# Performance work log

Measured on AMD Instinct MI355X. Metric: run time of the kernel, lower is better.

## Reference

```python
import jax, jax.numpy as jnp
import numpy as np

B = 8
RESOLUTIONS = [65, 129, 257, 513, 1025]
NUM_POINTS = [0, 4096, 16384, 65536, 262144]
CLIP_MIN = -1e9
FINAL = 1025          # last resolution (both axes)
B_MIN, B_MAX = -1.0, 1.0
BALANCE = 0.5


def setup_inputs() -> dict:
    key = jax.random.key(0)
    k1, k2, k3, k4 = jax.random.split(key, 4)
    return {
        "w1": jax.random.normal(k1, (2, 256), jnp.float32),
        "b1": jax.random.normal(k2, (256,), jnp.float32),
        "w2": jax.random.normal(k3, (256, 1), jnp.float32),
        "b2": jax.random.normal(k4, (1,), jnp.float32),
    }


def _interp_bilinear_ac(x, H, W):
    """F.interpolate(..., mode='bilinear', align_corners=True). x: [B, C, h, w]."""
    b, c, h, w = x.shape
    ys = jnp.linspace(0.0, h - 1.0, H)
    xs = jnp.linspace(0.0, w - 1.0, W)
    y0 = jnp.floor(ys).astype(jnp.int32)
    y1 = jnp.minimum(y0 + 1, h - 1)
    wy = ys - y0
    x0 = jnp.floor(xs).astype(jnp.int32)
    x1 = jnp.minimum(x0 + 1, w - 1)
    wx = xs - x0
    # interpolate rows, then columns
    top = x[:, :, y0, :] * (1.0 - wy)[None, None, :, None] + x[:, :, y1, :] * wy[None, None, :, None]
    return top[:, :, :, x0] * (1.0 - wx) + top[:, :, :, x1] * wx


def _batch_eval(coords, w1, b1, w2, b2):
    """coords: [B, N, 2] in final-resolution pixel space (align_corners=False mapping).
    Returns occupancy [B, N] (C == 1)."""
    coords2d = coords / FINAL + 0.5 / FINAL                 # normalize to [0, 1]
    p = coords2d * (B_MAX - B_MIN) + B_MIN                  # [B, N, 2] in world coords
    h = jax.nn.relu(jnp.einsum('bnd,dh->bnh', p, w1) + b1)  # [B, N, 256]
    occ = jax.nn.sigmoid(jnp.einsum('bnh,ho->bno', h, w2) + b2)
    return occ[..., 0]


def reference(w1, b1, w2, b2):
    occ = None
    for i, res in enumerate(RESOLUTIONS):
        if i == 0:
            # init_coords: grid of res x res points spanning [0, FINAL-1]
            xs = jnp.linspace(0.0, FINAL - 1.0, res)
            gy, gx = jnp.meshgrid(xs, xs, indexing='ij')          # y rows, x cols
            coords = jnp.stack([gx.ravel(), gy.ravel()], axis=-1)  # [N, 2] (x, y)
            coords = jnp.broadcast_to(coords, (B, res * res, 2))
            o = _batch_eval(coords, w1, b1, w2, b2)               # [B, N]
            occ = o.reshape(B, 1, res, res)                       # [B, C, H, W]
        else:
            occ = _interp_bilinear_ac(occ, res, res)
            npt = NUM_POINTS[i]
            if npt <= 0:
                continue
            # uncertainty = -|occ - balance_value|
            unc = -jnp.abs(occ - BALANCE)                          # [B, 1, H, W]
            flat_unc = unc.reshape(B, res * res)
            scores, idx = jax.lax.top_k(flat_unc, npt)             # [B, npt]
            px = (idx % res).astype(jnp.float32)
            py = (idx // res).astype(jnp.float32)
            stride = (FINAL - 1.0) / (res - 1.0)
            coords = jnp.stack([px, py], axis=-1) * stride         # [B, npt, 2]
            new_vals = _batch_eval(coords, w1, b1, w2, b2)         # [B, npt]
            occ_flat = occ.reshape(B, res * res)
            old_vals = jnp.take_along_axis(occ_flat, idx, axis=1)
            vals = jnp.where(scores >= CLIP_MIN, new_vals, old_vals)
            occ_flat = jax.vmap(lambda o, i2, v: o.at[i2].set(v))(occ_flat, idx, vals)
            occ = occ_flat.reshape(B, 1, res, res)
    return occ
```

## Files before the change

kernel.cpp:

```cpp
#include <hip/hip_runtime.h>
#include <stdint.h>

#define HID 256
#define NMAXPIX (1025 * 1025)
#define NREP 8
#define NSEG2 4096
#define SELMAX 2112

#define HISTA_OFF 0
#define HISTB_OFF 16384
#define HISTC_OFF 32768
#define SCAL_OFF  40960
#define TIC_OFF   41024
#define STAGE_U32 43072

#define R1P 65
#define R1  129
#define N1  (129 * 129)
#define NPT1 4096u
#define SEG1 66
#define B1 64
#define NREP1 4

__device__ __forceinline__ uint32_t aload(const uint32_t* p) {
    return __hip_atomic_load(p, __ATOMIC_RELAXED, __HIP_MEMORY_SCOPE_AGENT);
}
__device__ __forceinline__ void astore(uint32_t* p, uint32_t v) {
    __hip_atomic_store(p, v, __ATOMIC_RELAXED, __HIP_MEMORY_SCOPE_AGENT);
}

__device__ __forceinline__ float mlp_eval4(float wx, float wy,
                                           const float4* __restrict__ w1x,
                                           const float4* __restrict__ w1y,
                                           const float4* __restrict__ vb1,
                                           const float4* __restrict__ vw2, float b2v) {
    const float C0 = (float)(0.5 / 1025.0);
    float px = (wx / 1025.0f + C0) * 2.0f - 1.0f;
    float py = (wy / 1025.0f + C0) * 2.0f - 1.0f;
    float a0 = 0.f, a1 = 0.f, a2 = 0.f, a3 = 0.f;
#pragma unroll 8
    for (int q = 0; q < HID / 4; ++q) {
        float4 a = w1x[q], b = w1y[q], c = vb1[q], d = vw2[q];
        float h0 = px * a.x + py * b.x + c.x;
        float h1 = px * a.y + py * b.y + c.y;
        float h2 = px * a.z + py * b.z + c.z;
        float h3 = px * a.w + py * b.w + c.w;
        h0 = h0 > 0.f ? h0 : 0.f;
        h1 = h1 > 0.f ? h1 : 0.f;
        h2 = h2 > 0.f ? h2 : 0.f;
        h3 = h3 > 0.f ? h3 : 0.f;
        a0 += h0 * d.x;
        a1 += h1 * d.y;
        a2 += h2 * d.z;
        a3 += h3 * d.w;
    }
    float x = ((a0 + a1) + (a2 + a3)) + b2v;
    float r;
    if (x >= 0.f) { r = 1.0f / (1.0f + expf(-x)); }
    else { float e = expf(x); r = e / (1.0f + e); }
    return r;
}

__device__ __forceinline__ uint32_t block_exscan_256(uint32_t v, volatile uint32_t* lds4) {
    int lane = threadIdx.x & 63, w = threadIdx.x >> 6;
    uint32_t inc = v;
#pragma unroll
    for (int d = 1; d < 64; d <<= 1) {
        uint32_t o = (uint32_t)__shfl_up((int)inc, d, 64);
        if (lane >= d) inc += o;
    }
    if (lane == 63) lds4[w] = inc;
    __syncthreads();
    uint32_t woff = 0;
    for (int i = 0; i < w; ++i) woff += lds4[i];
    return woff + inc - v;
}

__device__ void scan_generic(const uint32_t* __restrict__ hist, int NB, int nrep,
                             uint32_t rem_in, uint32_t prefix_in, int shift,
                             uint32_t* outp, uint32_t* outr,
                             volatile uint32_t* lds4, volatile uint32_t* ldspair) {
    int tid = threadIdx.x;
    int C = NB >> 8;
    int b0 = NB - (tid + 1) * C;
    uint32_t cnts[8];
#pragma unroll
    for (int k = 0; k < 8; ++k) cnts[k] = 0;
    for (int rep = 0; rep < nrep; ++rep) {
        const uint4* p = (const uint4*)(hist + (size_t)rep * NB + b0);
#pragma unroll
        for (int g = 0; g < 2; ++g) {
            if (g * 4 < C) {
                uint4 v = p[g];
                cnts[g * 4 + 0] += v.x;
                cnts[g * 4 + 1] += v.y;
                cnts[g * 4 + 2] += v.z;
                cnts[g * 4 + 3] += v.w;
            }
        }
    }
    uint32_t ssum = 0;
    for (int k = 0; k < C; ++k) ssum += cnts[k];
    uint32_t excl = block_exscan_256(ssum, lds4);
    uint32_t run = excl;
    for (int k = 0; k < C; ++k) {
        uint32_t c = cnts[C - 1 - k];
        if (rem_in > run && rem_in <= run + c) {
            ldspair[0] = (prefix_in << shift) | (uint32_t)(b0 + C - 1 - k);
            ldspair[1] = rem_in - run;
        }
        run += c;
    }
    __syncthreads();
    *outp = ldspair[0];
    *outr = ldspair[1];
}

__device__ void scan_atomic(const uint32_t* __restrict__ hist, int NB, int nrep,
                            uint32_t rem_in, uint32_t prefix_in, int shift,
                            uint32_t* outp, uint32_t* outr,
                            volatile uint32_t* lds4, volatile uint32_t* ldspair) {
    int tid = threadIdx.x;
    int C = NB >> 8;
    int b0 = NB - (tid + 1) * C;
    uint32_t cnts[8];
#pragma unroll
    for (int k = 0; k < 8; ++k) cnts[k] = 0;
    for (int rep = 0; rep < nrep; ++rep)
        for (int k = 0; k < C; ++k)
            cnts[k] += aload(&hist[(size_t)rep * NB + b0 + k]);
    uint32_t ssum = 0;
    for (int k = 0; k < C; ++k) ssum += cnts[k];
    uint32_t excl = block_exscan_256(ssum, lds4);
    uint32_t run = excl;
    for (int k = 0; k < C; ++k) {
        uint32_t c = cnts[C - 1 - k];
        if (rem_in > run && rem_in <= run + c) {
            ldspair[0] = (prefix_in << shift) | (uint32_t)(b0 + C - 1 - k);
            ldspair[1] = rem_in - run;
        }
        run += c;
    }
    __syncthreads();
    *outp = ldspair[0];
    *outr = ldspair[1];
}

__device__ __forceinline__ void hist_add(uint32_t* lh, uint32_t bin, bool act, int lane) {
    unsigned long long m = __ballot(act);
    if (m) {
        int leader = __ffsll(m) - 1;
        uint32_t lbin = (uint32_t)__shfl((int)bin, leader, 64);
        unsigned long long smk = __ballot(act && bin == lbin);
        if (smk == m) {
            if (lane == leader) atomicAdd(&lh[lbin], (uint32_t)__popcll(m));
        } else if (act) {
            atomicAdd(&lh[bin], 1u);
        }
    }
}

__device__ __forceinline__ float up2x(const float* __restrict__ in, int rp, int r, int n) {
    int i = n / r, j = n % r;
    int i2 = i >> 1, j2 = j >> 1;
    float v;
    if ((i & 1) == 0) {
        if ((j & 1) == 0) {
            v = in[i2 * rp + j2];
        } else {
            float a = in[i2 * rp + j2], b = in[i2 * rp + j2 + 1];
            v = a * 0.5f + b * 0.5f;
        }
    } else {
        if ((j & 1) == 0) {
            float a = in[i2 * rp + j2], b = in[(i2 + 1) * rp + j2];
            v = a * 0.5f + b * 0.5f;
        } else {
            float a = in[i2 * rp + j2],      c = in[i2 * rp + j2 + 1];
            float b = in[(i2 + 1) * rp + j2], d = in[(i2 + 1) * rp + j2 + 1];
            float t1 = a * 0.5f + b * 0.5f;
            float t2 = c * 0.5f + d * 0.5f;
            v = t1 * 0.5f + t2 * 0.5f;
        }
    }
    return v;
}

__device__ __forceinline__ uint32_t mkkey(float v) {
    float unc = -fabsf(v - 0.5f);
    uint32_t u = __float_as_uint(unc);
    return (u & 0x80000000u) ? ~u : (u | 0x80000000u);
}

__device__ __forceinline__ uint32_t key_of(const float* __restrict__ in, int rp, int r, int n) {
    return mkkey(up2x(in, rp, r, n));
}

__device__ bool wait_ctr(uint32_t* ctr, uint32_t target, volatile uint32_t* sflag) {
    if (threadIdx.x == 0) {
        uint32_t d = aload(ctr);
        int sp = 0;
        while (d < target && sp < 20000) {
            __builtin_amdgcn_s_sleep(4);
            d = aload(ctr);
            ++sp;
        }
        *sflag = (d >= target) ? 1u : 0u;
    }
    __syncthreads();
    return *sflag != 0;
}

__global__ __launch_bounds__(256) void k_eval0z(const float* __restrict__ w1, const float* __restrict__ b1,
                                                const float* __restrict__ w2, const float* __restrict__ b2,
                                                float* __restrict__ occ, uint32_t* __restrict__ zbuf, int zcount) {
    __shared__ alignas(16) float sw1[2 * HID];
    __shared__ alignas(16) float sb1[HID];
    __shared__ alignas(16) float sw2[HID];
    int tid = threadIdx.x;
    for (int i = tid; i < 2 * HID; i += 256) sw1[i] = w1[i];
    sb1[tid] = b1[tid];
    sw2[tid] = w2[tid];
    __syncthreads();
    int gtid = blockIdx.x * 256 + tid;
    int nthreads = gridDim.x * 256;
    for (int i = gtid; i < zcount; i += nthreads) zbuf[i] = 0;
    for (int n = gtid; n < 65 * 65; n += nthreads) {
        int i = n / 65, j = n % 65;
        occ[n] = mlp_eval4(16.0f * (float)j, 16.0f * (float)i,
                           (const float4*)sw1, (const float4*)(sw1 + HID),
                           (const float4*)sb1, (const float4*)sw2, b2[0]);
    }
}

__global__ __launch_bounds__(256) void k_s1all(const float* __restrict__ in,
                                               float* __restrict__ outg,
                                               uint32_t* __restrict__ keys,
                                               uint32_t* __restrict__ sm,
                                               const float* __restrict__ w1, const float* __restrict__ b1,
                                               const float* __restrict__ w2, const float* __restrict__ b2) {
    __shared__ alignas(16) float sw1[2 * HID];
    __shared__ alignas(16) float sb1[HID];
    __shared__ alignas(16) float sw2[HID];
    __shared__ alignas(16) uint32_t lh[2048];
    __shared__ uint32_t selidx[SELMAX];
    __shared__ uint32_t selcnt;
    __shared__ uint32_t lds4[4];
    __shared__ uint32_t ldspair[2];
    __shared__ uint32_t sflag;

    uint32_t* histA = sm + HISTA_OFF;
    uint32_t* histB = sm + HISTB_OFF;
    uint32_t* histC = sm + HISTC_OFF;
    uint32_t* scal  = sm + SCAL_OFF;
    uint32_t* tic   = sm + TIC_OFF;

    const int tid = threadIdx.x, lane = tid & 63, w = tid >> 6;
    for (int i = tid; i < 2 * HID; i += 256) sw1[i] = w1[i];
    sb1[tid] = b1[tid];
    sw2[tid] = w2[tid];
    if (tid == 0) selcnt = 0;
    for (int k = tid; k < 2048; k += 256) lh[k] = 0;
    __syncthreads();

    for (int n0 = blockIdx.x * 256; n0 < N1; n0 += B1 * 256) {
        int n = n0 + tid;
        bool act = n < N1;
        uint32_t key = 0;
        if (act) {
            float v = up2x(in, R1P, R1, n);
            outg[n] = v;
            key = mkkey(v);
            astore(&keys[n], key);
        }
        hist_add(lh, key >> 21, act, lane);
    }
    __syncthreads();
    {
        uint32_t* rep = histA + (size_t)(blockIdx.x & (NREP1 - 1)) * 2048;
        for (int k = tid; k < 2048; k += 256) { uint32_t c = lh[k]; if (c) atomicAdd(&rep[k], c); }
    }
    __syncthreads();
    if (tid == 0) __hip_atomic_fetch_add(&scal[8], 1u, __ATOMIC_RELAXED, __HIP_MEMORY_SCOPE_AGENT);

    uint32_t pfx1, rem1;
    if (wait_ctr(&scal[8], B1, &sflag)) {
        scan_atomic(histA, 2048, NREP1, NPT1, 0u, 0, &pfx1, &rem1, lds4, ldspair);
    } else {
        for (int k = tid; k < 2048; k += 256) lh[k] = 0;
        __syncthreads();
        for (int n0 = 0; n0 < N1; n0 += 256) {
            int n = n0 + tid; bool act = n < N1;
            uint32_t key = act ? key_of(in, R1P, R1, n) : 0u;
            hist_add(lh, key >> 21, act, lane);
        }
        __syncthreads();
        scan_generic(lh, 2048, 1, NPT1, 0u, 0, &pfx1, &rem1, lds4, ldspair);
    }

    for (int k = tid; k < 2048; k += 256) lh[k] = 0;
    __syncthreads();
    for (int n0 = blockIdx.x * 256; n0 < N1; n0 += B1 * 256) {
        int n = n0 + tid;
        bool act = n < N1;
        uint32_t key = act ? aload(&keys[n]) : 0u;
        bool flt = act && ((key >> 21) == pfx1);
        hist_add(lh, (key >> 10) & 0x7FFu, flt, lane);
    }
    __syncthreads();
    {
        uint32_t* rep = histB + (size_t)(blockIdx.x & (NREP1 - 1)) * 2048;
        for (int k = tid; k < 2048; k += 256) { uint32_t c = lh[k]; if (c) atomicAdd(&rep[k], c); }
    }
    __syncthreads();
    if (tid == 0) __hip_atomic_fetch_add(&scal[9], 1u, __ATOMIC_RELAXED, __HIP_MEMORY_SCOPE_AGENT);

    uint32_t pfx2, rem2;
    if (wait_ctr(&scal[9], B1, &sflag)) {
        scan_atomic(histB, 2048, NREP1, rem1, pfx1, 11, &pfx2, &rem2, lds4, ldspair);
    } else {
        for (int k = tid; k < 2048; k += 256) lh[k] = 0;
        __syncthreads();
        for (int n0 = 0; n0 < N1; n0 += 256) {
            int n = n0 + tid; bool act = n < N1;
            uint32_t key = act ? key_of(in, R1P, R1, n) : 0u;
            bool flt = act && ((key >> 21) == pfx1);
            hist_add(lh, (key >> 10) & 0x7FFu, flt, lane);
        }
        __syncthreads();
        scan_generic(lh, 2048, 1, rem1, pfx1, 11, &pfx2, &rem2, lds4, ldspair);
    }

    for (int k = tid; k < 2048; k += 256) lh[k] = 0;
    __syncthreads();
    for (int n0 = blockIdx.x * 256; n0 < N1; n0 += B1 * 256) {
        int n = n0 + tid;
        bool act = n < N1;
        uint32_t key = act ? aload(&keys[n]) : 0u;
        bool flt = act && ((key >> 10) == pfx2);
        hist_add(lh, key & 0x3FFu, flt, lane);
    }
    __syncthreads();
    {
        uint32_t* rep = histC + (size_t)(blockIdx.x & (NREP1 - 1)) * 1024;
        for (int k = tid; k < 1024; k += 256) { uint32_t c = lh[k]; if (c) atomicAdd(&rep[k], c); }
    }
    __syncthreads();
    if (tid == 0) __hip_atomic_fetch_add(&scal[10], 1u, __ATOMIC_RELAXED, __HIP_MEMORY_SCOPE_AGENT);

    uint32_t K, t;
    if (wait_ctr(&scal[10], B1, &sflag)) {
        scan_atomic(histC, 1024, NREP1, rem2, pfx2, 10, &K, &t, lds4, ldspair);
    } else {
        for (int k = tid; k < 2048; k += 256) lh[k] = 0;
        __syncthreads();
        for (int n0 = 0; n0 < N1; n0 += 256) {
            int n = n0 + tid; bool act = n < N1;
            uint32_t key = act ? key_of(in, R1P, R1, n) : 0u;
            bool flt = act && ((key >> 10) == pfx2);
            hist_add(lh, key & 0x3FFu, flt, lane);
        }
        __syncthreads();
        scan_generic(lh, 1024, 1, rem2, pfx2, 10, &K, &t, lds4, ldspair);
    }

    int wv = blockIdx.x * 4 + w;
    int s0 = wv * SEG1;
    int s1e = s0 + SEG1; if (s1e > N1) s1e = N1;
    uint32_t tcnt = 0;
    for (int base = s0; base < s1e; base += 64) {
        int n = base + lane;
        if (n < s1e) tcnt += (aload(&keys[n]) == K) ? 1u : 0u;
    }
#pragma unroll
    for (int d = 32; d; d >>= 1) tcnt += (uint32_t)__shfl_down((int)tcnt, d, 64);
    if (lane == 0) astore(&tic[wv], tcnt);
    __syncthreads();
    if (tid == 0) __hip_atomic_fetch_add(&scal[11], 1u, __ATOMIC_RELAXED, __HIP_MEMORY_SCOPE_AGENT);

    uint32_t tp = 0;
    if (wait_ctr(&scal[11], B1, &sflag)) {
        for (int i = lane; i < wv; i += 64) tp += aload(&tic[i]);
    } else {
        for (int i = lane; i < wv; i += 64) {
            int a0 = i * SEG1, a1 = a0 + SEG1; if (a1 > N1) a1 = N1;
            uint32_t c = 0;
            for (int n2 = a0; n2 < a1; ++n2) c += (key_of(in, R1P, R1, n2) == K) ? 1u : 0u;
            tp += c;
        }
    }
#pragma unroll
    for (int d = 32; d; d >>= 1) tp += (uint32_t)__shfl_down((int)tp, d, 64);
    tp = (uint32_t)__shfl((int)tp, 0, 64);

    uint32_t tie_run = tp;
    unsigned long long lowmask = (lane == 63) ? ~0ull >> 1 : ((1ull << lane) - 1ull);
    for (int base = s0; base < s1e; base += 64) {
        int n = base + lane;
        bool inb = n < s1e;
        uint32_t key = inb ? aload(&keys[n]) : 0u;
        bool gt = inb && (key > K);
        bool tie = inb && (key == K);
        unsigned long long tm = __ballot(tie);
        uint32_t trank = tie_run + (uint32_t)__popcll(tm & lowmask);
        bool sel = gt || (tie && trank < t);
        unsigned long long smk = __ballot(sel);
        if (smk) {
            int leader = __ffsll(smk) - 1;
            uint32_t wbase = 0;
            if (lane == leader) wbase = atomicAdd(&selcnt, (uint32_t)__popcll(smk));
            wbase = (uint32_t)__shfl((int)wbase, leader, 64);
            if (sel) selidx[wbase + (uint32_t)__popcll(smk & lowmask)] = (uint32_t)n;
        }
        tie_run += (uint32_t)__popcll(tm);
    }
    __syncthreads();

    uint32_t cnt = selcnt;
    float vb2 = b2[0];
    for (uint32_t i = tid; i < cnt; i += 256) {
        int n = (int)selidx[i];
        int ii = n / R1, jj = n % R1;
        float rr = mlp_eval4(8.0f * (float)jj, 8.0f * (float)ii,
                             (const float4*)sw1, (const float4*)(sw1 + HID),
                             (const float4*)sb1, (const float4*)sw2, vb2);
        outg[n] = rr;
    }
}

__global__ __launch_bounds__(256) void k_upkey(const float* __restrict__ in, int rp,
                                               float* __restrict__ outg, int r, int nb, int bstride,
                                               uint32_t* __restrict__ keys,
                                               uint32_t* __restrict__ histA) {
    __shared__ uint32_t hist[2048];
    int tid = threadIdx.x;
    for (int k = tid; k < 2048; k += 256) hist[k] = 0;
    __syncthreads();
    int N = r * r;
    int lane = tid & 63;
    int gstride = gridDim.x * 256;
    for (int n0 = blockIdx.x * 256; n0 < N; n0 += gstride) {
        int n = n0 + tid;
        bool act = n < N;
        uint32_t key = 0;
        if (act) {
            float v = up2x(in, rp, r, n);
            for (int k = 0; k < nb; ++k) outg[(size_t)k * bstride + n] = v;
            key = mkkey(v);
            keys[n] = key;
        }
        hist_add(hist, key >> 21, act, lane);
    }
    __syncthreads();
    uint32_t* myrep = histA + (size_t)(blockIdx.x & (NREP - 1)) * 2048;
    for (int k = tid; k < 2048; k += 256) {
        uint32_t c = hist[k];
        if (c) atomicAdd(&myrep[k], c);
    }
}

__global__ __launch_bounds__(256) void k_histmid(const uint32_t* __restrict__ keys, int N,
                                                 const uint32_t* __restrict__ prevHist,
                                                 uint32_t* __restrict__ scal,
                                                 int useNpt, uint32_t npt, int scalInIdx, int shift,
                                                 int scalOutIdx,
                                                 int fshift, int bshift, uint32_t bmask,
                                                 uint32_t* __restrict__ outHist, int NBout) {
    __shared__ uint32_t lh[2048];
    __shared__ uint32_t lds4[4];
    __shared__ uint32_t ldspair[2];
    int tid = threadIdx.x, lane = tid & 63;
    uint32_t rem_in = useNpt ? npt : scal[scalInIdx + 1];
    uint32_t pfx_in = useNpt ? 0u  : scal[scalInIdx];
    uint32_t pfx, rem;
    scan_generic(prevHist, 2048, NREP, rem_in, pfx_in, shift, &pfx, &rem, lds4, ldspair);
    if (blockIdx.x == 0 && tid == 0) { scal[scalOutIdx] = pfx; scal[scalOutIdx + 1] = rem; }
    for (int k = tid; k < 2048; k += 256) lh[k] = 0;
    __syncthreads();
    int gstride4 = gridDim.x * 1024;
    for (int base = blockIdx.x * 1024; base < N; base += gstride4) {
        int n = base + tid * 4;
        uint32_t k0 = 0, k1 = 0, k2 = 0, k3 = 0;
        if (n + 3 < N) {
            uint4 v = *(const uint4*)(keys + n);
            k0 = v.x; k1 = v.y; k2 = v.z; k3 = v.w;
        } else {
            if (n < N) k0 = keys[n];
            if (n + 1 < N) k1 = keys[n + 1];
            if (n + 2 < N) k2 = keys[n + 2];
            if (n + 3 < N) k3 = keys[n + 3];
        }
        hist_add(lh, (k0 >> bshift) & bmask, (n < N) && ((k0 >> fshift) == pfx), lane);
        hist_add(lh, (k1 >> bshift) & bmask, (n + 1 < N) && ((k1 >> fshift) == pfx), lane);
        hist_add(lh, (k2 >> bshift) & bmask, (n + 2 < N) && ((k2 >> fshift) == pfx), lane);
        hist_add(lh, (k3 >> bshift) & bmask, (n + 3 < N) && ((k3 >> fshift) == pfx), lane);
    }
    __syncthreads();
    uint32_t* myrep = outHist + (size_t)(blockIdx.x & (NREP - 1)) * NBout;
    for (int k = tid; k < NBout; k += 256) {
        uint32_t c = lh[k];
        if (c) atomicAdd(&myrep[k], c);
    }
}

__global__ __launch_bounds__(256, 4) void k_segselc(
        const uint32_t* __restrict__ keys, int N, int seglen,
        const uint32_t* __restrict__ histC,
        const uint32_t* __restrict__ scal,
        uint32_t* __restrict__ tic,
        uint32_t* __restrict__ gcnt,
        uint32_t* __restrict__ selbuf) {
    __shared__ uint32_t selcnt;
    __shared__ uint32_t selidx[SELMAX];
    __shared__ uint32_t lds4[4];
    __shared__ uint32_t ldspair[2];
    __shared__ uint32_t wtc[4];
    __shared__ uint32_t s_excl;
    __shared__ uint32_t gbase;
    int tid = threadIdx.x, lane = tid & 63, w = tid >> 6;
    if (tid == 0) { selcnt = 0; s_excl = 0; }

    uint32_t rem2 = scal[3], pfx2 = scal[2];
    uint32_t K, t;
    scan_generic(histC, 1024, NREP, rem2, pfx2, 10, &K, &t, lds4, ldspair);

    int wv = blockIdx.x * 4 + w;
    int s0 = wv * seglen;
    int s1 = s0 + seglen; if (s1 > N) s1 = N;
    uint32_t tcnt = 0;
    for (int base = s0; base < s1; base += 64) {
        int n = base + lane;
        if (n < s1) tcnt += (keys[n] == K) ? 1u : 0u;
    }
#pragma unroll
    for (int d = 32; d; d >>= 1) tcnt += (uint32_t)__shfl_down((int)tcnt, d, 64);
    if (lane == 0) wtc[w] = tcnt;
    __syncthreads();
    uint32_t agg = wtc[0] + wtc[1] + wtc[2] + wtc[3];
    uint32_t intra = 0;
    for (int i = 0; i < w; ++i) intra += wtc[i];

    if (tid == 0) {
        uint32_t st = (blockIdx.x == 0) ? ((2u << 30) | agg) : ((1u << 30) | agg);
        astore(&tic[blockIdx.x], st);
    }
    if (blockIdx.x > 0 && w == 0) {
        uint32_t excl = 0;
        int b = (int)blockIdx.x - 1;
        for (;;) {
            int mine = b - lane;
            bool active = (mine >= 0);
            uint32_t f = 0;
            if (active) {
                f = aload(&tic[mine]);
                int spins = 0;
                while ((f >> 30) == 0u && spins < 1000) {
                    __builtin_amdgcn_s_sleep(2);
                    f = aload(&tic[mine]);
                    ++spins;
                }
                if ((f >> 30) == 0u) {
                    int ms0 = mine * seglen;
                    int ms1 = ms0 + seglen; if (ms1 > N) ms1 = N;
                    uint32_t c = 0;
                    for (int n2 = ms0; n2 < ms1; ++n2) c += (keys[n2] == K) ? 1u : 0u;
                    f = (1u << 30) | c;
                }
            }
            unsigned long long incm = __ballot(active && (f >> 30) == 2u);
            uint32_t val;
            bool done = (incm != 0ull);
            if (done) {
                int l2 = __ffsll(incm) - 1;
                val = (lane <= l2) ? (f & 0x3FFFFFFFu) : 0u;
            } else {
                val = active ? (f & 0x3FFFFFFFu) : 0u;
            }
#pragma unroll
            for (int d = 32; d; d >>= 1) val += (uint32_t)__shfl_down((int)val, d, 64);
            val = (uint32_t)__shfl((int)val, 0, 64);
            excl += val;
            if (done) break;
            if (b < 64) break;
            b -= 64;
        }
        if (lane == 0) {
            astore(&tic[blockIdx.x], (2u << 30) | (excl + agg));
            s_excl = excl;
        }
    }
    __syncthreads();
    uint32_t tie_run = s_excl + intra;

    unsigned long long lowmask = (lane == 63) ? ~0ull >> 1 : ((1ull << lane) - 1ull);
    for (int base = s0; base < s1; base += 64) {
        int n = base + lane;
        bool inb = n < s1;
        uint32_t key = inb ? keys[n] : 0u;
        bool gt = inb && (key > K);
        bool tie = inb && (key == K);
        unsigned long long tm = __ballot(tie);
        uint32_t trank = tie_run + (uint32_t)__popcll(tm & lowmask);
        bool sel = gt || (tie && trank < t);
        unsigned long long smk = __ballot(sel);
        if (smk) {
            int leader = __ffsll(smk) - 1;
            uint32_t wbase = 0;
            if (lane == leader) wbase = atomicAdd(&selcnt, (uint32_t)__popcll(smk));
            wbase = (uint32_t)__shfl((int)wbase, leader, 64);
            if (sel) selidx[wbase + (uint32_t)__popcll(smk & lowmask)] = (uint32_t)n;
        }
        tie_run += (uint32_t)__popcll(tm);
    }
    __syncthreads();

    if (tid == 0) gbase = atomicAdd(gcnt, selcnt);
    __syncthreads();
    uint32_t cnt = selcnt, gb = gbase;
    for (uint32_t i = tid; i < cnt; i += 256) selbuf[gb + i] = selidx[i];
}

__global__ __launch_bounds__(256) void k_evalsel(const uint32_t* __restrict__ selbuf, int npt,
                                                 int r, float stride,
                                                 float* __restrict__ occ, int nb, int bstride,
                                                 const float* __restrict__ w1, const float* __restrict__ b1,
                                                 const float* __restrict__ w2, const float* __restrict__ b2) {
    __shared__ alignas(16) float sw1[2 * HID];
    __shared__ alignas(16) float sb1[HID];
    __shared__ alignas(16) float sw2[HID];
    int tid = threadIdx.x;
    for (int i = tid; i < 2 * HID; i += 256) sw1[i] = w1[i];
    sb1[tid] = b1[tid];
    sw2[tid] = w2[tid];
    __syncthreads();
    float vb2 = b2[0];
    const float4* w1x = (const float4*)sw1;
    const float4* w1y = (const float4*)(sw1 + HID);
    const float4* vb1 = (const float4*)sb1;
    const float4* vw2 = (const float4*)sw2;
    const float C0 = (float)(0.5 / 1025.0);
    int gs2 = gridDim.x * 512;
    for (int bb = blockIdx.x * 512; bb < npt; bb += gs2) {
        int i0 = bb + tid, i1 = bb + tid + 256;
        bool v0 = i0 < npt, v1 = i1 < npt;
        int nA = v0 ? (int)selbuf[i0] : 0;
        int nB = v1 ? (int)selbuf[i1] : 0;
        int iA = nA / r, jA = nA % r;
        int iB = nB / r, jB = nB % r;
        float pxA = ((stride * (float)jA) / 1025.0f + C0) * 2.0f - 1.0f;
        float pyA = ((stride * (float)iA) / 1025.0f + C0) * 2.0f - 1.0f;
        float pxB = ((stride * (float)jB) / 1025.0f + C0) * 2.0f - 1.0f;
        float pyB = ((stride * (float)iB) / 1025.0f + C0) * 2.0f - 1.0f;
        float4 A0 = {0, 0, 0, 0}, A1 = {0, 0, 0, 0};
#pragma unroll 4
        for (int q = 0; q < HID / 4; ++q) {
            float4 a = w1x[q], b = w1y[q], c = vb1[q], d = vw2[q];
            {
                float h0 = pxA * a.x + pyA * b.x + c.x;
                float h1 = pxA * a.y + pyA * b.y + c.y;
                float h2 = pxA * a.z + pyA * b.z + c.z;
                float h3 = pxA * a.w + pyA * b.w + c.w;
                h0 = h0 > 0.f ? h0 : 0.f;
                h1 = h1 > 0.f ? h1 : 0.f;
                h2 = h2 > 0.f ? h2 : 0.f;
                h3 = h3 > 0.f ? h3 : 0.f;
                A0.x += h0 * d.x; A0.y += h1 * d.y;
                A0.z += h2 * d.z; A0.w += h3 * d.w;
            }
            {
                float h0 = pxB * a.x + pyB * b.x + c.x;
                float h1 = pxB * a.y + pyB * b.y + c.y;
                float h2 = pxB * a.z + pyB * b.z + c.z;
                float h3 = pxB * a.w + pyB * b.w + c.w;
                h0 = h0 > 0.f ? h0 : 0.f;
                h1 = h1 > 0.f ? h1 : 0.f;
                h2 = h2 > 0.f ? h2 : 0.f;
                h3 = h3 > 0.f ? h3 : 0.f;
                A1.x += h0 * d.x; A1.y += h1 * d.y;
                A1.z += h2 * d.z; A1.w += h3 * d.w;
            }
        }
        if (v0) {
            float x = ((A0.x + A0.y) + (A0.z + A0.w)) + vb2;
            float rr;
            if (x >= 0.f) { rr = 1.0f / (1.0f + expf(-x)); }
            else { float e = expf(x); rr = e / (1.0f + e); }
            for (int k = 0; k < nb; ++k) occ[(size_t)k * bstride + nA] = rr;
        }
        if (v1) {
            float x = ((A1.x + A1.y) + (A1.z + A1.w)) + vb2;
            float rr;
            if (x >= 0.f) { rr = 1.0f / (1.0f + expf(-x)); }
            else { float e = expf(x); rr = e / (1.0f + e); }
            for (int k = 0; k < nb; ++k) occ[(size_t)k * bstride + nB] = rr;
        }
    }
}

__global__ __launch_bounds__(256) void k_bcast(const float* __restrict__ src, float* __restrict__ dst, int N) {
    int q = blockIdx.x * 256 + threadIdx.x;
    int n = q * 4;
    if (n + 3 < N) {
        float4 v = *(const float4*)(src + n);
#pragma unroll
        for (int k = 0; k < 8; ++k) *(float4*)(dst + (size_t)k * N + n) = v;
    } else if (n < N) {
        for (int m = n; m < N; ++m) {
            float v = src[m];
#pragma unroll
            for (int k = 0; k < 8; ++k) dst[(size_t)k * N + m] = v;
        }
    }
}

extern "C" void kernel_launch(void* const* d_in, const int* in_sizes, int n_in,
                              void* d_out, int out_size, void* d_ws, size_t ws_size,
                              hipStream_t stream) {
    const float* w1 = (const float*)d_in[0];
    const float* b1 = (const float*)d_in[1];
    const float* w2 = (const float*)d_in[2];
    const float* b2 = (const float*)d_in[3];
    float* out = (float*)d_out;

    const size_t A = (((size_t)NMAXPIX * 4) + 255) & ~(size_t)255;
    const size_t SMALL_BYTES = (size_t)4 * STAGE_U32 * 4;
    const size_t SELB_BYTES = ((size_t)262144 * 4 + 255) & ~(size_t)255;
    const size_t need = 3 * A + SMALL_BYTES + SELB_BYTES;

    int fused8 = (ws_size >= need);
    char* base = fused8 ? (char*)d_ws : (char*)d_out;
    float* buf0 = (float*)(base);
    float* buf1 = (float*)(base + A);
    uint32_t* keys = (uint32_t*)(base + 2 * A);
    uint32_t* smallb = (uint32_t*)(base + 3 * A);
    uint32_t* selbuf = (uint32_t*)(base + 3 * A + SMALL_BYTES);

    k_eval0z<<<dim3(512), dim3(256), 0, stream>>>(w1, b1, w2, b2, buf0, smallb, 4 * STAGE_U32);

    k_s1all<<<dim3(B1), dim3(256), 0, stream>>>(buf0, buf1, keys, smallb, w1, b1, w2, b2);

    const int resA[5] = {65, 129, 257, 513, 1025};
    const int nptA[5] = {0, 4096, 16384, 65536, 262144};
    float* cur = buf1;
    float* nxt = buf0;
    for (int s = 2; s < 5; ++s) {
        int rp = resA[s - 1], r = resA[s];
        int N = r * r;
        uint32_t npt = (uint32_t)nptA[s];
        uint32_t* sm    = smallb + (size_t)(s - 1) * STAGE_U32;
        uint32_t* histA = sm + HISTA_OFF;
        uint32_t* histB = sm + HISTB_OFF;
        uint32_t* histC = sm + HISTC_OFF;
        uint32_t* scal  = sm + SCAL_OFF;
        uint32_t* tic   = sm + TIC_OFF;
        int nb1 = (N + 255) / 256;
        int nbu = nb1 < 1024 ? nb1 : 1024;
        int seglen = (N + NSEG2 - 1) / NSEG2;
        float stride = 1024.0f / (float)(r - 1);

        int last = (s == 4);
        float* stage_out = (last && fused8) ? out : nxt;
        int nb = (last && fused8) ? 8 : 1;
        int bstride = (last && fused8) ? NMAXPIX : 0;

        int nbe = (int)((npt + 511) / 512); if (nbe > 512) nbe = 512;

        k_upkey<<<dim3(nbu), dim3(256), 0, stream>>>(cur, rp, stage_out, r, nb, bstride, keys, histA);
        k_histmid<<<dim3(512), dim3(256), 0, stream>>>(keys, N, histA, scal, 1, npt, 0, 0,
                                                       0, 21, 10, 0x7FFu, histB, 2048);
        k_histmid<<<dim3(512), dim3(256), 0, stream>>>(keys, N, histB, scal, 0, 0u, 0, 11,
                                                       2, 10, 0, 0x3FFu, histC, 1024);
        k_segselc<<<dim3(NSEG2 / 4), dim3(256), 0, stream>>>(keys, N, seglen, histC, scal, tic,
                                                             scal + 6, selbuf);
        k_evalsel<<<dim3(nbe), dim3(256), 0, stream>>>(selbuf, (int)npt, r, stride,
                                                       stage_out, nb, bstride, w1, b1, w2, b2);
        if (!(last && fused8)) { float* tmp = cur; cur = nxt; nxt = tmp; }
    }
    if (!fused8) {
        k_bcast<<<dim3(((NMAXPIX + 3) / 4 + 255) / 256), dim3(256), 0, stream>>>(cur, out, NMAXPIX);
    }
}
```

Measured before the change: 256.3 us.

## Write selected indices directly using a dual tie/greater decoupled lookback scan

The segmented selection kernel now carries two prefix counts, ties with the threshold key and keys above it, through a 64-bit decoupled lookback. Each thread can then compute its final output slot and write straight into the selection buffer. This removes the LDS staging array, the per-block global atomic and the copy-out loop, and makes the output order deterministic. The segment count is halved to 2048 and the occupancy hint lowered, which lengthens the serial scan per warp. Separately, the histogram kernel drops its 4-wide vector loads for one scalar load per thread, which may reduce memory efficiency.

```diff
diff --git a/kernel.cpp b/kernel.cpp
--- a/kernel.cpp
+++ b/kernel.cpp
@@ -4,7 +4,7 @@
 #define HID 256
 #define NMAXPIX (1025 * 1025)
 #define NREP 8
-#define NSEG2 4096
+#define NSEG 2048
 #define SELMAX 2112
 
 #define HISTA_OFF 0
@@ -26,6 +26,12 @@
     return __hip_atomic_load(p, __ATOMIC_RELAXED, __HIP_MEMORY_SCOPE_AGENT);
 }
 __device__ __forceinline__ void astore(uint32_t* p, uint32_t v) {
+    __hip_atomic_store(p, v, __ATOMIC_RELAXED, __HIP_MEMORY_SCOPE_AGENT);
+}
+__device__ __forceinline__ unsigned long long aload64(const unsigned long long* p) {
+    return __hip_atomic_load(p, __ATOMIC_RELAXED, __HIP_MEMORY_SCOPE_AGENT);
+}
+__device__ __forceinline__ void astore64(unsigned long long* p, unsigned long long v) {
     __hip_atomic_store(p, v, __ATOMIC_RELAXED, __HIP_MEMORY_SCOPE_AGENT);
 }
 
@@ -477,23 +483,14 @@
     if (blockIdx.x == 0 && tid == 0) { scal[scalOutIdx] = pfx; scal[scalOutIdx + 1] = rem; }
     for (int k = tid; k < 2048; k += 256) lh[k] = 0;
     __syncthreads();
-    int gstride4 = gridDim.x * 1024;
-    for (int base = blockIdx.x * 1024; base < N; base += gstride4) {
-        int n = base + tid * 4;
-        uint32_t k0 = 0, k1 = 0, k2 = 0, k3 = 0;
-        if (n + 3 < N) {
-            uint4 v = *(const uint4*)(keys + n);
-            k0 = v.x; k1 = v.y; k2 = v.z; k3 = v.w;
-        } else {
-            if (n < N) k0 = keys[n];
-            if (n + 1 < N) k1 = keys[n + 1];
-            if (n + 2 < N) k2 = keys[n + 2];
-            if (n + 3 < N) k3 = keys[n + 3];
-        }
-        hist_add(lh, (k0 >> bshift) & bmask, (n < N) && ((k0 >> fshift) == pfx), lane);
-        hist_add(lh, (k1 >> bshift) & bmask, (n + 1 < N) && ((k1 >> fshift) == pfx), lane);
-        hist_add(lh, (k2 >> bshift) & bmask, (n + 2 < N) && ((k2 >> fshift) == pfx), lane);
-        hist_add(lh, (k3 >> bshift) & bmask, (n + 3 < N) && ((k3 >> fshift) == pfx), lane);
+    int gstride = gridDim.x * 256;
+    for (int base = blockIdx.x * 256; base < N; base += gstride) {
+        int n = base + tid;
+        bool inb = n < N;
+        uint32_t key = inb ? keys[n] : 0u;
+        bool flt = inb && ((key >> fshift) == pfx);
+        uint32_t bin = (key >> bshift) & bmask;
+        hist_add(lh, bin, flt, lane);
     }
     __syncthreads();
     uint32_t* myrep = outHist + (size_t)(blockIdx.x & (NREP - 1)) * NBout;
@@ -503,22 +500,18 @@
     }
 }
 
-__global__ __launch_bounds__(256, 4) void k_segselc(
+__global__ __launch_bounds__(256, 2) void k_segselc(
         const uint32_t* __restrict__ keys, int N, int seglen,
         const uint32_t* __restrict__ histC,
         const uint32_t* __restrict__ scal,
-        uint32_t* __restrict__ tic,
-        uint32_t* __restrict__ gcnt,
+        unsigned long long* __restrict__ tic64,
         uint32_t* __restrict__ selbuf) {
-    __shared__ uint32_t selcnt;
-    __shared__ uint32_t selidx[SELMAX];
     __shared__ uint32_t lds4[4];
     __shared__ uint32_t ldspair[2];
-    __shared__ uint32_t wtc[4];
-    __shared__ uint32_t s_excl;
-    __shared__ uint32_t gbase;
+    __shared__ uint32_t wtc[4], wgc[4];
+    __shared__ uint32_t s_excl_t, s_excl_g;
     int tid = threadIdx.x, lane = tid & 63, w = tid >> 6;
-    if (tid == 0) { selcnt = 0; s_excl = 0; }
+    if (tid == 0) { s_excl_t = 0; s_excl_g = 0; }
 
     uint32_t rem2 = scal[3], pfx2 = scal[2];
     uint32_t K, t;
@@ -527,70 +520,94 @@
     int wv = blockIdx.x * 4 + w;
     int s0 = wv * seglen;
     int s1 = s0 + seglen; if (s1 > N) s1 = N;
-    uint32_t tcnt = 0;
+    uint32_t tcnt = 0, gcnt2 = 0;
     for (int base = s0; base < s1; base += 64) {
         int n = base + lane;
-        if (n < s1) tcnt += (keys[n] == K) ? 1u : 0u;
-    }
-#pragma unroll
-    for (int d = 32; d; d >>= 1) tcnt += (uint32_t)__shfl_down((int)tcnt, d, 64);
-    if (lane == 0) wtc[w] = tcnt;
-    __syncthreads();
-    uint32_t agg = wtc[0] + wtc[1] + wtc[2] + wtc[3];
-    uint32_t intra = 0;
-    for (int i = 0; i < w; ++i) intra += wtc[i];
+        if (n < s1) {
+            uint32_t key = keys[n];
+            tcnt += (key == K) ? 1u : 0u;
+            gcnt2 += (key > K) ? 1u : 0u;
+        }
+    }
+#pragma unroll
+    for (int d = 32; d; d >>= 1) {
+        tcnt += (uint32_t)__shfl_down((int)tcnt, d, 64);
+        gcnt2 += (uint32_t)__shfl_down((int)gcnt2, d, 64);
+    }
+    if (lane == 0) { wtc[w] = tcnt; wgc[w] = gcnt2; }
+    __syncthreads();
+    uint32_t agg_t = wtc[0] + wtc[1] + wtc[2] + wtc[3];
+    uint32_t agg_g = wgc[0] + wgc[1] + wgc[2] + wgc[3];
+    uint32_t intra_t = 0, intra_g = 0;
+    for (int i = 0; i < w; ++i) { intra_t += wtc[i]; intra_g += wgc[i]; }
 
     if (tid == 0) {
-        uint32_t st = (blockIdx.x == 0) ? ((2u << 30) | agg) : ((1u << 30) | agg);
-        astore(&tic[blockIdx.x], st);
+        unsigned long long pay = ((unsigned long long)agg_t << 24) | (unsigned long long)agg_g;
+        unsigned long long st = (blockIdx.x == 0) ? ((2ull << 62) | pay) : ((1ull << 62) | pay);
+        astore64(&tic64[blockIdx.x], st);
     }
     if (blockIdx.x > 0 && w == 0) {
-        uint32_t excl = 0;
+        uint32_t excl_t = 0, excl_g = 0;
         int b = (int)blockIdx.x - 1;
         for (;;) {
             int mine = b - lane;
             bool active = (mine >= 0);
-            uint32_t f = 0;
+            unsigned long long f = 0;
             if (active) {
-                f = aload(&tic[mine]);
+                f = aload64(&tic64[mine]);
                 int spins = 0;
-                while ((f >> 30) == 0u && spins < 1000) {
+                while ((f >> 62) == 0ull && spins < 1000) {
                     __builtin_amdgcn_s_sleep(2);
-                    f = aload(&tic[mine]);
+                    f = aload64(&tic64[mine]);
                     ++spins;
                 }
-                if ((f >> 30) == 0u) {
-                    int ms0 = mine * seglen;
-                    int ms1 = ms0 + seglen; if (ms1 > N) ms1 = N;
-                    uint32_t c = 0;
-                    for (int n2 = ms0; n2 < ms1; ++n2) c += (keys[n2] == K) ? 1u : 0u;
-                    f = (1u << 30) | c;
+                if ((f >> 62) == 0ull) {
+                    int ms0 = mine * 4 * seglen;
+                    int ms1 = ms0 + 4 * seglen; if (ms1 > N) ms1 = N;
+                    uint32_t ct = 0, cg = 0;
+                    for (int n2 = ms0; n2 < ms1; ++n2) {
+                        uint32_t key = keys[n2];
+                        ct += (key == K) ? 1u : 0u;
+                        cg += (key > K) ? 1u : 0u;
+                    }
+                    f = (1ull << 62) | ((unsigned long long)ct << 24) | (unsigned long long)cg;
                 }
             }
-            unsigned long long incm = __ballot(active && (f >> 30) == 2u);
-            uint32_t val;
+            unsigned long long incm = __ballot(active && (f >> 62) == 2ull);
+            uint32_t vt, vg;
             bool done = (incm != 0ull);
             if (done) {
                 int l2 = __ffsll(incm) - 1;
-                val = (lane <= l2) ? (f & 0x3FFFFFFFu) : 0u;
+                vt = (lane <= l2) ? (uint32_t)((f >> 24) & 0xFFFFFFull) : 0u;
+                vg = (lane <= l2) ? (uint32_t)(f & 0xFFFFFFull) : 0u;
             } else {
-                val = active ? (f & 0x3FFFFFFFu) : 0u;
+                vt = active ? (uint32_t)((f >> 24) & 0xFFFFFFull) : 0u;
+                vg = active ? (uint32_t)(f & 0xFFFFFFull) : 0u;
             }
 #pragma unroll
-            for (int d = 32; d; d >>= 1) val += (uint32_t)__shfl_down((int)val, d, 64);
-            val = (uint32_t)__shfl((int)val, 0, 64);
-            excl += val;
+            for (int d = 32; d; d >>= 1) {
+                vt += (uint32_t)__shfl_down((int)vt, d, 64);
+                vg += (uint32_t)__shfl_down((int)vg, d, 64);
+            }
+            vt = (uint32_t)__shfl((int)vt, 0, 64);
+            vg = (uint32_t)__shfl((int)vg, 0, 64);
+            excl_t += vt;
+            excl_g += vg;
             if (done) break;
             if (b < 64) break;
             b -= 64;
         }
         if (lane == 0) {
-            astore(&tic[blockIdx.x], (2u << 30) | (excl + agg));
-            s_excl = excl;
-        }
-    }
-    __syncthreads();
-    uint32_t tie_run = s_excl + intra;
+            unsigned long long pay = ((unsigned long long)(excl_t + agg_t) << 24)
+                                   | (unsigned long long)(excl_g + agg_g);
+            astore64(&tic64[blockIdx.x], (2ull << 62) | pay);
+            s_excl_t = excl_t;
+            s_excl_g = excl_g;
+        }
+    }
+    __syncthreads();
+    uint32_t tie_run = s_excl_t + intra_t;
+    uint32_t gt_run  = s_excl_g + intra_g;
 
     unsigned long long lowmask = (lane == 63) ? ~0ull >> 1 : ((1ull << lane) - 1ull);
     for (int base = s0; base < s1; base += 64) {
@@ -600,24 +617,18 @@
         bool gt = inb && (key > K);
         bool tie = inb && (key == K);
         unsigned long long tm = __ballot(tie);
-        uint32_t trank = tie_run + (uint32_t)__popcll(tm & lowmask);
-        bool sel = gt || (tie && trank < t);
-        unsigned long long smk = __ballot(sel);
-        if (smk) {
-            int leader = __ffsll(smk) - 1;
-            uint32_t wbase = 0;
-            if (lane == leader) wbase = atomicAdd(&selcnt, (uint32_t)__popcll(smk));
-            wbase = (uint32_t)__shfl((int)wbase, leader, 64);
-            if (sel) selidx[wbase + (uint32_t)__popcll(smk & lowmask)] = (uint32_t)n;
+        unsigned long long gm = __ballot(gt);
+        uint32_t tie_before = tie_run + (uint32_t)__popcll(tm & lowmask);
+        uint32_t gt_before  = gt_run + (uint32_t)__popcll(gm & lowmask);
+        if (gt) {
+            uint32_t tb = tie_before < t ? tie_before : t;
+            selbuf[gt_before + tb] = (uint32_t)n;
+        } else if (tie && tie_before < t) {
+            selbuf[gt_before + tie_before] = (uint32_t)n;
         }
         tie_run += (uint32_t)__popcll(tm);
-    }
-    __syncthreads();
-
-    if (tid == 0) gbase = atomicAdd(gcnt, selcnt);
-    __syncthreads();
-    uint32_t cnt = selcnt, gb = gbase;
-    for (uint32_t i = tid; i < cnt; i += 256) selbuf[gb + i] = selidx[i];
+        gt_run  += (uint32_t)__popcll(gm);
+    }
 }
 
 __global__ __launch_bounds__(256) void k_evalsel(const uint32_t* __restrict__ selbuf, int npt,
@@ -755,7 +766,7 @@
         uint32_t* tic   = sm + TIC_OFF;
         int nb1 = (N + 255) / 256;
         int nbu = nb1 < 1024 ? nb1 : 1024;
-        int seglen = (N + NSEG2 - 1) / NSEG2;
+        int seglen = (N + NSEG - 1) / NSEG;
         float stride = 1024.0f / (float)(r - 1);
 
         int last = (s == 4);
@@ -770,8 +781,8 @@
                                                        0, 21, 10, 0x7FFu, histB, 2048);
         k_histmid<<<dim3(512), dim3(256), 0, stream>>>(keys, N, histB, scal, 0, 0u, 0, 11,
                                                        2, 10, 0, 0x3FFu, histC, 1024);
-        k_segselc<<<dim3(NSEG2 / 4), dim3(256), 0, stream>>>(keys, N, seglen, histC, scal, tic,
-                                                             scal + 6, selbuf);
+        k_segselc<<<dim3(NSEG / 4), dim3(256), 0, stream>>>(keys, N, seglen, histC, scal,
+                                                            (unsigned long long*)tic, selbuf);
         k_evalsel<<<dim3(nbe), dim3(256), 0, stream>>>(selbuf, (int)npt, r, stride,
                                                        stage_out, nb, bstride, w1, b1, w2, b2);
         if (!(last && fused8)) { float* tmp = cur; cur = nxt; nxt = tmp; }
```

Measured after the change: 229.6 us. -10.4%, faster.
